# Kernel tuning notes

Hardware: AMD Instinct MI355X
Metric: run time of the kernel (lower is better)

The kernel has to match this reference:

```python
import jax, jax.numpy as jnp
import numpy as np

BS, N, NP, K = 2, 4096, 1024, 8   # batch, fine pts, coarse pts, in-degree per fine node
CI, CO, MID = 32, 16, 32          # in channels (16 skip + 16 interpolated), out channels, radial MLP width
E = BS * N * K


def setup_inputs() -> dict:
    key = jax.random.key(0)
    ks = iter(jax.random.split(key, 64))
    nrm = lambda s, sc=1.0: jax.random.normal(next(ks), s, jnp.float32) * sc
    inp = {}
    inp['h0'] = nrm((BS * N, 16, 1))
    inp['h1'] = nrm((BS * N, 16, 3))
    inp['uph0'] = nrm((BS * NP, 16, 1))
    inp['uph1'] = nrm((BS * NP, 16, 3))
    inp['xyz'] = jax.random.uniform(next(ks), (BS, N, 3), jnp.float32)
    inp['xyz_prev'] = jax.random.uniform(next(ks), (BS, NP, 3), jnp.float32)
    dst = jnp.repeat(jnp.arange(BS * N, dtype=jnp.int32), K)
    src = (dst // N) * N + jax.random.randint(next(ks), (E,), 0, N, jnp.int32)
    inp['edge_src'], inp['edge_dst'] = src, dst
    xf = inp['xyz'].reshape(BS * N, 3)
    inp['r'] = jnp.linalg.norm(xf[src] - xf[dst], axis=-1, keepdims=True)
    # CG basis tensors basis[din,dout]: [E, 2*dout+1, 2*din+1, 2*min(din,dout)+1]
    inp['basis00'] = nrm((E, 1, 1, 1))
    inp['basis01'] = nrm((E, 3, 1, 1))
    inp['basis10'] = nrm((E, 1, 3, 1))
    inp['basis11'] = nrm((E, 3, 3, 3))
    for p, f in (('00', 1), ('01', 1), ('10', 1), ('11', 3)):
        inp['rw1_' + p] = nrm((1, MID), 0.5)
        inp['rb1_' + p] = jnp.zeros((MID,), jnp.float32)
        inp['rw2_' + p] = nrm((MID, MID), 0.2)
        inp['rb2_' + p] = jnp.zeros((MID,), jnp.float32)
        inp['rw3_' + p] = nrm((MID, CO * CI * f), 0.1)
    inp['wself0'] = nrm((CO, CI), 0.1)
    inp['wself1'] = nrm((CO, CI), 0.1)
    inp['gamma0'] = jnp.ones((CO,), jnp.float32)
    inp['beta0'] = jnp.zeros((CO,), jnp.float32)
    inp['gamma1'] = jnp.ones((CO,), jnp.float32)
    inp['beta1'] = jnp.zeros((CO,), jnp.float32)
    return inp


def _radial(r, w1, b1, w2, b2, w3, f):
    x = jax.nn.relu(r @ w1 + b1)
    x = jax.nn.relu(x @ w2 + b2)
    return (x @ w3).reshape(E, CO, CI, f)


def _pair_msg(basis, hsrc, R):
    # basis [E,mo,mi,f], hsrc [E,ci,mi], R [E,co,ci,f] -> msg [E,co,mo]
    # (fused form of per-edge kernel = sum_f R*basis followed by kernel @ src)
    tmp = jnp.einsum('emnf,ein->eimf', basis, hsrc)
    return jnp.einsum('eoif,eimf->eom', R, tmp)


def _gnorm(h, gamma, beta):
    # GNormSE3: norm over m-dim, LayerNorm+ReLU on norms, rescale phase
    n = jnp.sqrt(jnp.sum(h * h, -1) + 1e-12)           # [Nn,co]
    phase = h / n[..., None]
    mu = jnp.mean(n, -1, keepdims=True)
    var = jnp.var(n, -1, keepdims=True)
    t = jax.nn.relu((n - mu) / jnp.sqrt(var + 1e-5) * gamma + beta)
    return t[..., None] * phase


def _fwd(h0, h1, uph0, uph1, xyz, xyz_prev, r, basis00, basis01, basis10, basis11,
         rw1_00, rb1_00, rw2_00, rb2_00, rw3_00,
         rw1_01, rb1_01, rw2_01, rb2_01, rw3_01,
         rw1_10, rb1_10, rw2_10, rb2_10, rw3_10,
         rw1_11, rb1_11, rw2_11, rb2_11, rw3_11,
         wself0, wself1, gamma0, beta0, gamma1, beta1, edge_src, edge_dst):
    # --- three_nn + inverse-squared-distance interpolation of coarse features ---
    d2 = jnp.sum((xyz[:, :, None, :] - xyz_prev[:, None, :, :]) ** 2, -1)  # [B,N,NP]
    negd, idx = jax.lax.top_k(-d2, 3)
    dist = jnp.sqrt(jnp.maximum(-negd, 0.0))
    d2c = jnp.maximum(dist * dist, 1e-10)
    inv = 1.0 / (d2c + 1e-8)
    w = inv / jnp.sum(inv, -1, keepdims=True)          # [B,N,3]

    def interp(uph):
        C, F = uph.shape[1], uph.shape[2]
        fp = uph.reshape(BS, NP, C * F)
        g = jax.vmap(lambda f_, i_: f_[i_])(fp, idx)   # [B,N,3,C*F]
        return jnp.sum(g * w[..., None], 2).reshape(BS * N, C, F)

    h0c = jnp.concatenate([interp(uph0), h0], 1)       # [BN,CI,1]
    h1c = jnp.concatenate([interp(uph1), h1], 1)       # [BN,CI,3]

    # --- GConvSE3: per-edge CG-basis kernels, mean aggregation, self-interaction ---
    hs0, hs1 = h0c[edge_src], h1c[edge_src]
    R00 = _radial(r, rw1_00, rb1_00, rw2_00, rb2_00, rw3_00, 1)
    R01 = _radial(r, rw1_01, rb1_01, rw2_01, rb2_01, rw3_01, 1)
    R10 = _radial(r, rw1_10, rb1_10, rw2_10, rb2_10, rw3_10, 1)
    R11 = _radial(r, rw1_11, rb1_11, rw2_11, rb2_11, rw3_11, 3)
    msg0 = _pair_msg(basis00, hs0, R00) + _pair_msg(basis10, hs1, R10)  # [E,CO,1]
    msg1 = _pair_msg(basis01, hs0, R01) + _pair_msg(basis11, hs1, R11)  # [E,CO,3]
    agg0 = jax.ops.segment_sum(msg0, edge_dst, num_segments=BS * N) / K  # mean (in-degree K)
    agg1 = jax.ops.segment_sum(msg1, edge_dst, num_segments=BS * N) / K
    out0 = agg0 + jnp.einsum('oi,nim->nom', wself0, h0c)
    out1 = agg1 + jnp.einsum('oi,nim->nom', wself1, h1c)

    return _gnorm(out0, gamma0, beta0), _gnorm(out1, gamma1, beta1)


def reference(h0, h1, uph0, uph1, xyz, xyz_prev, r, basis00, basis01, basis10, basis11,
              rw1_00, rb1_00, rw2_00, rb2_00, rw3_00,
              rw1_01, rb1_01, rw2_01, rb2_01, rw3_01,
              rw1_10, rb1_10, rw2_10, rb2_10, rw3_10,
              rw1_11, rb1_11, rw2_11, rb2_11, rw3_11,
              wself0, wself1, gamma0, beta0, gamma1, beta1, edge_src, edge_dst):
    return _fwd(h0, h1, uph0, uph1, xyz, xyz_prev, r, basis00, basis01, basis10, basis11,
                rw1_00, rb1_00, rw2_00, rb2_00, rw3_00,
                rw1_01, rb1_01, rw2_01, rb2_01, rw3_01,
                rw1_10, rb1_10, rw2_10, rb2_10, rw3_10,
                rw1_11, rb1_11, rw2_11, rb2_11, rw3_11,
                wself0, wself1, gamma0, beta0, gamma1, beta1, edge_src, edge_dst)
```

## Files before the change

### kernel.cpp

```cpp
#include <hip/hip_runtime.h>
#include <hip/hip_bf16.h>
#include <hip/hip_fp16.h>
#include <math.h>

#define NPP   1024
#define BN    8192
#define NE    65536

typedef __attribute__((ext_vector_type(8))) short bf16x8;
typedef __attribute__((ext_vector_type(4))) float f32x4;

__device__ __forceinline__ short f2bf(float f) {
  __hip_bfloat16 h = __float2bfloat16(f);
  return *reinterpret_cast<short*>(&h);
}
__device__ __forceinline__ float b2f(short h) {
  unsigned u = ((unsigned)(unsigned short)h) << 16;
  return __uint_as_float(u);
}
__device__ __forceinline__ unsigned short f2h(float f) {
  __half h = __float2half(f);
  return *reinterpret_cast<unsigned short*>(&h);
}
__device__ __forceinline__ float h2f(unsigned short u) {
  __half h = *reinterpret_cast<__half*>(&u);
  return __half2float(h);
}

__device__ __forceinline__ unsigned long long pkkey(float d, int j) {
  return ((unsigned long long)__float_as_uint(d) << 32) | (unsigned int)j;
}

__global__ __launch_bounds__(256) void prolog_kernel(
    const float* __restrict__ h0, const float* __restrict__ h1,
    const float* __restrict__ uph0, const float* __restrict__ uph1,
    const float* __restrict__ xyz, const float* __restrict__ xyzp,
    float* __restrict__ h0c, float* __restrict__ h1c,
    const float* __restrict__ w00, const float* __restrict__ w01,
    const float* __restrict__ w10, const float* __restrict__ w11,
    const float* __restrict__ w2_00, const float* __restrict__ w2_01,
    const float* __restrict__ w2_10, const float* __restrict__ w2_11,
    unsigned short* __restrict__ B00, unsigned short* __restrict__ B01,
    unsigned short* __restrict__ B10, unsigned short* __restrict__ B11,
    unsigned short* __restrict__ W2H, unsigned short* __restrict__ W2L)
{
  const int tid = threadIdx.x;
  if (blockIdx.x >= BN/4) {
    int idx = (blockIdx.x - BN/4) * 256 + tid;
    if (idx < 49152) {
      int a = idx & 16383;
      int i = a & 31, o = (a >> 5) & 15, k = a >> 9;
      int src = k*512 + o*32 + i;
      if (idx < 16384)      B00[a] = (unsigned short)f2bf(w00[src]);
      else if (idx < 32768) B01[a] = (unsigned short)f2bf(w01[src]);
      else                  B10[a] = (unsigned short)f2bf(w10[src]);
    } else if (idx < 98304) {
      int a = idx - 49152;
      int i = a & 31, o = (a >> 5) & 15, s = a >> 9;
      int f = s >> 5, k = s & 31;
      B11[a] = (unsigned short)f2bf(w11[k*1536 + (o*32+i)*3 + f]);
    } else if (idx < 102400) {
      int a = idx - 98304;
      int p = a >> 10, rem = a & 1023;
      int b = rem >> 5, aa = rem & 31;
      const float* w2p = p==0?w2_00 : p==1?w2_01 : p==2?w2_10 : w2_11;
      W2H[a] = (unsigned short)f2bf(w2p[aa*32 + b]);
    } else if (idx < 106496) {
      int a = idx - 102400;
      int p = a >> 10, rem = a & 1023;
      int b = rem >> 5, aa = rem & 31;
      const float* w2p = p==0?w2_00 : p==1?w2_01 : p==2?w2_10 : w2_11;
      float v = w2p[aa*32 + b];
      short h = f2bf(v);
      W2L[a] = (unsigned short)f2bf(v - b2f(h));
    }
    return;
  }

  const int lane = tid & 63;
  const int wid  = tid >> 6;
  const int fi   = blockIdx.x * 4 + wid;
  const int b    = fi >> 12;

  const float px = xyz[fi*3+0], py = xyz[fi*3+1], pz = xyz[fi*3+2];

  unsigned long long k0 = ~0ull, k1 = ~0ull, k2 = ~0ull;
  const float* cbase = xyzp + (size_t)b*NPP*3;
  #pragma unroll 4
  for (int j = lane; j < NPP; j += 64) {
    const float* cp = cbase + j*3;
    float ax = px - cp[0], ay = py - cp[1], az = pz - cp[2];
    float dd = fmaf(az, az, fmaf(ay, ay, ax*ax));
    unsigned long long kk = pkkey(dd, j);
    if (kk < k0)      { k2 = k1; k1 = k0; k0 = kk; }
    else if (kk < k1) { k2 = k1; k1 = kk; }
    else if (kk < k2) { k2 = kk; }
  }
  #pragma unroll
  for (int off = 1; off < 64; off <<= 1) {
    unsigned long long b0 = __shfl_xor(k0, off);
    unsigned long long b1 = __shfl_xor(k1, off);
    unsigned long long b2 = __shfl_xor(k2, off);
    unsigned long long c0, c1, c2;
    if (k0 <= b0) {
      c0 = k0;
      if (k1 <= b0) { c1 = k1; c2 = (k2 <= b0) ? k2 : b0; }
      else          { c1 = b0; c2 = (k1 <= b1) ? k1 : b1; }
    } else {
      c0 = b0;
      if (b1 <= k0) { c1 = b1; c2 = (b2 <= k0) ? b2 : k0; }
      else          { c1 = k0; c2 = (b1 <= k1) ? b1 : k1; }
    }
    k0 = c0; k1 = c1; k2 = c2;
  }
  const int i0 = (int)(k0 & 0xffffffffu);
  const int i1 = (int)(k1 & 0xffffffffu);
  const int i2 = (int)(k2 & 0xffffffffu);
  const float dd0 = __uint_as_float((unsigned)(k0 >> 32));
  const float dd1 = __uint_as_float((unsigned)(k1 >> 32));
  const float dd2 = __uint_as_float((unsigned)(k2 >> 32));

  float w0, w1v, w2v;
  {
    float s0 = sqrtf(fmaxf(dd0, 0.f));
    float s1 = sqrtf(fmaxf(dd1, 0.f));
    float s2 = sqrtf(fmaxf(dd2, 0.f));
    w0  = 1.f / (fmaxf(s0*s0, 1e-10f) + 1e-8f);
    w1v = 1.f / (fmaxf(s1*s1, 1e-10f) + 1e-8f);
    w2v = 1.f / (fmaxf(s2*s2, 1e-10f) + 1e-8f);
    float wsum = w0 + w1v + w2v;
    w0 /= wsum; w1v /= wsum; w2v /= wsum;
  }

  const float* u0 = uph0 + (size_t)b*NPP*16;
  const float* u1 = uph1 + (size_t)b*NPP*48;
  if (lane < 16) {
    int c = lane;
    h0c[(size_t)fi*32 + c] = w0*u0[i0*16+c] + w1v*u0[i1*16+c] + w2v*u0[i2*16+c];
    h0c[(size_t)fi*32 + 16 + c] = h0[(size_t)fi*16 + c];
  } else {
    int q = lane - 16;
    h1c[(size_t)fi*96 + q] = w0*u1[i0*48+q] + w1v*u1[i1*48+q] + w2v*u1[i2*48+q];
    h1c[(size_t)fi*96 + 48 + q] = h1[(size_t)fi*48 + q];
  }
}

struct EP {
  const float *r; const int *esrc;
  const float *b00, *b01, *b10, *b11;
  const float *w1_00, *b1_00, *b2_00;
  const float *w1_01, *b1_01, *b2_01;
  const float *w1_10, *b1_10, *b2_10;
  const float *w1_11, *b1_11, *b2_11;
  const unsigned short *B00, *B01, *B10, *B11, *W2H, *W2L;
  const float *h0c, *h1c;
  float *agg0, *agg1;
};

#define CVT4(PTR) ({ ushort4 u_ = *(const ushort4*)(PTR); \
    f32x4 r_; r_[0]=h2f(u_.x); r_[1]=h2f(u_.y); r_[2]=h2f(u_.z); r_[3]=h2f(u_.w); r_; })

__global__ __launch_bounds__(256) void edge_mfma(EP P)
{
  __shared__ __align__(16) unsigned short x2Lh[32*264];

  const int tid  = threadIdx.x;
  const int wid  = tid >> 6;
  const int lane = tid & 63;
  const int el   = lane & 15;
  const int kg   = lane >> 4;
  const int kg4  = kg << 2;
  const int eb   = blockIdx.x * 64 + wid * 16;
  const int e    = eb + el;
  const int isl  = kg * 8;

  const int   sidx = P.esrc[e];
  const float rv   = P.r[e];

  const f32x4 zero4 = {0.f, 0.f, 0.f, 0.f};

  #pragma unroll
  for (int p = 0; p < 4; ++p) {
    const float* w1p = p==0?P.w1_00 : p==1?P.w1_01 : p==2?P.w1_10 : P.w1_11;
    const float* b1p = p==0?P.b1_00 : p==1?P.b1_01 : p==2?P.b1_10 : P.b1_11;
    const float* b2p = p==0?P.b2_00 : p==1?P.b2_01 : p==2?P.b2_10 : P.b2_11;
    const unsigned short* w2hp = P.W2H + p*1024;
    const unsigned short* w2lp = P.W2L + p*1024;
    f32x4 wa  = *(const f32x4*)(w1p + isl);
    f32x4 wb  = *(const f32x4*)(w1p + isl + 4);
    f32x4 ba  = *(const f32x4*)(b1p + isl);
    f32x4 bbv = *(const f32x4*)(b1p + isl + 4);
    bf16x8 bh0 = *(const bf16x8*)(w2hp + el*32 + isl);
    bf16x8 bh1 = *(const bf16x8*)(w2hp + (16+el)*32 + isl);
    bf16x8 bl0 = *(const bf16x8*)(w2lp + el*32 + isl);
    bf16x8 bl1 = *(const bf16x8*)(w2lp + (16+el)*32 + isl);
    float b2v0 = b2p[el];
    float b2v1 = b2p[16 + el];
    bf16x8 axh, axl;
    #pragma unroll
    for (int j = 0; j < 4; ++j) {
      float v0 = fmaxf(fmaf(rv, wa[j], ba[j]),  0.f);
      float v1 = fmaxf(fmaf(rv, wb[j], bbv[j]), 0.f);
      short h0s = f2bf(v0), h1s_ = f2bf(v1);
      axh[j]   = h0s;  axl[j]   = f2bf(v0 - b2f(h0s));
      axh[j+4] = h1s_; axl[j+4] = f2bf(v1 - b2f(h1s_));
    }
    f32x4 z0 = __builtin_amdgcn_mfma_f32_16x16x32_bf16(axl, bh0, zero4, 0,0,0);
    z0 = __builtin_amdgcn_mfma_f32_16x16x32_bf16(axh, bl0, z0, 0,0,0);
    z0 = __builtin_amdgcn_mfma_f32_16x16x32_bf16(axh, bh0, z0, 0,0,0);
    f32x4 z1 = __builtin_amdgcn_mfma_f32_16x16x32_bf16(axl, bh1, zero4, 0,0,0);
    z1 = __builtin_amdgcn_mfma_f32_16x16x32_bf16(axh, bl1, z1, 0,0,0);
    z1 = __builtin_amdgcn_mfma_f32_16x16x32_bf16(axh, bh1, z1, 0,0,0);
    ushort4 o0, o1v;
    o0.x  = f2h(fmaxf(z0[0] + b2v0, 0.f));
    o0.y  = f2h(fmaxf(z0[1] + b2v0, 0.f));
    o0.z  = f2h(fmaxf(z0[2] + b2v0, 0.f));
    o0.w  = f2h(fmaxf(z0[3] + b2v0, 0.f));
    o1v.x = f2h(fmaxf(z1[0] + b2v1, 0.f));
    o1v.y = f2h(fmaxf(z1[1] + b2v1, 0.f));
    o1v.z = f2h(fmaxf(z1[2] + b2v1, 0.f));
    o1v.w = f2h(fmaxf(z1[3] + b2v1, 0.f));
    *(ushort4*)&x2Lh[el*264      + wid*64 + p*16 + kg4] = o0;
    *(ushort4*)&x2Lh[(16+el)*264 + wid*64 + p*16 + kg4] = o1v;
  }

  f32x4 h0a = *(const f32x4*)(P.h0c + (size_t)sidx*32 + isl);
  f32x4 h0b = *(const f32x4*)(P.h0c + (size_t)sidx*32 + isl + 4);
  float h1sl[24];
  {
    const float* hp = P.h1c + (size_t)sidx*96 + isl*3;
    #pragma unroll
    for (int q = 0; q < 6; ++q) {
      f32x4 v = *(const f32x4*)(hp + q*4);
      h1sl[q*4+0]=v[0]; h1sl[q*4+1]=v[1]; h1sl[q*4+2]=v[2]; h1sl[q*4+3]=v[3];
    }
  }

  bf16x8 a_h0;
  #pragma unroll
  for (int j = 0; j < 4; ++j) { a_h0[j] = f2bf(h0a[j]); a_h0[j+4] = f2bf(h0b[j]); }

  const int xrow = wid*64 + kg4;

  f32x4 macc0 = zero4;
  {
    const unsigned short* bb = P.B00 + el*32 + isl;
    #pragma unroll 4
    for (int t = 0; t < 32; ++t) {
      bf16x8 bv = *(const bf16x8*)(bb + t*512);
      f32x4 z = __builtin_amdgcn_mfma_f32_16x16x32_bf16(a_h0, bv, zero4, 0, 0, 0);
      f32x4 xs = CVT4(&x2Lh[t*264 + xrow + 0]);
      macc0[0] = fmaf(xs[0], z[0], macc0[0]);
      macc0[1] = fmaf(xs[1], z[1], macc0[1]);
      macc0[2] = fmaf(xs[2], z[2], macc0[2]);
      macc0[3] = fmaf(xs[3], z[3], macc0[3]);
    }
  }
  {
    f32x4 bv = *(const f32x4*)(P.b00 + eb + kg4);
    macc0[0]*=bv[0]; macc0[1]*=bv[1]; macc0[2]*=bv[2]; macc0[3]*=bv[3];
  }

  {
    const float* bp = P.b10 + (size_t)e*3;
    float c0 = bp[0], c1 = bp[1], c2 = bp[2];
    bf16x8 a_t;
    #pragma unroll
    for (int j = 0; j < 8; ++j)
      a_t[j] = f2bf(c0*h1sl[j*3+0] + c1*h1sl[j*3+1] + c2*h1sl[j*3+2]);
    const unsigned short* bb = P.B10 + el*32 + isl;
    #pragma unroll 4
    for (int t = 0; t < 32; ++t) {
      bf16x8 bv = *(const bf16x8*)(bb + t*512);
      f32x4 z = __builtin_amdgcn_mfma_f32_16x16x32_bf16(a_t, bv, zero4, 0, 0, 0);
      f32x4 xs = CVT4(&x2Lh[t*264 + xrow + 32]);
      macc0[0] = fmaf(xs[0], z[0], macc0[0]);
      macc0[1] = fmaf(xs[1], z[1], macc0[1]);
      macc0[2] = fmaf(xs[2], z[2], macc0[2]);
      macc0[3] = fmaf(xs[3], z[3], macc0[3]);
    }
  }
  {
    float s = macc0[0]+macc0[1]+macc0[2]+macc0[3];
    s += __shfl_xor(s, 16);
    if ((kg & 1) == 0)
      P.agg0[(size_t)((eb >> 3) + (kg >> 1))*16 + el] = s * 0.125f;
  }

  f32x4 c01 = zero4;
  {
    const unsigned short* bb = P.B01 + el*32 + isl;
    #pragma unroll 4
    for (int t = 0; t < 32; ++t) {
      bf16x8 bv = *(const bf16x8*)(bb + t*512);
      f32x4 z = __builtin_amdgcn_mfma_f32_16x16x32_bf16(a_h0, bv, zero4, 0, 0, 0);
      f32x4 xs = CVT4(&x2Lh[t*264 + xrow + 16]);
      c01[0] = fmaf(xs[0], z[0], c01[0]);
      c01[1] = fmaf(xs[1], z[1], c01[1]);
      c01[2] = fmaf(xs[2], z[2], c01[2]);
      c01[3] = fmaf(xs[3], z[3], c01[3]);
    }
  }
  f32x4 m1a, m1b, m1c;
  {
    const float* bp = P.b01 + (size_t)(eb + kg4)*3;
    f32x4 q0 = *(const f32x4*)(bp);
    f32x4 q1 = *(const f32x4*)(bp + 4);
    f32x4 q2 = *(const f32x4*)(bp + 8);
    m1a[0]=c01[0]*q0[0]; m1a[1]=c01[1]*q0[3]; m1a[2]=c01[2]*q1[2]; m1a[3]=c01[3]*q2[1];
    m1b[0]=c01[0]*q0[1]; m1b[1]=c01[1]*q1[0]; m1b[2]=c01[2]*q1[3]; m1b[3]=c01[3]*q2[2];
    m1c[0]=c01[0]*q0[2]; m1c[1]=c01[1]*q1[1]; m1c[2]=c01[2]*q2[0]; m1c[3]=c01[3]*q2[3];
  }

  {
    const float* b11e = P.b11 + (size_t)e*27;
    #pragma unroll 1
    for (int f = 0; f < 3; ++f) {
      float bm[9];
      #pragma unroll
      for (int mn = 0; mn < 9; ++mn) bm[mn] = b11e[mn*3 + f];
      bf16x8 am0, am1, am2;
      #pragma unroll
      for (int j = 0; j < 8; ++j) {
        float hn0 = h1sl[j*3+0], hn1 = h1sl[j*3+1], hn2 = h1sl[j*3+2];
        am0[j] = f2bf(bm[0]*hn0 + bm[1]*hn1 + bm[2]*hn2);
        am1[j] = f2bf(bm[3]*hn0 + bm[4]*hn1 + bm[5]*hn2);
        am2[j] = f2bf(bm[6]*hn0 + bm[7]*hn1 + bm[8]*hn2);
      }
      const unsigned short* bb = P.B11 + (size_t)f*16384 + el*32 + isl;
      #pragma unroll 4
      for (int t = 0; t < 32; ++t) {
        bf16x8 bv = *(const bf16x8*)(bb + t*512);
        f32x4 z0 = __builtin_amdgcn_mfma_f32_16x16x32_bf16(am0, bv, zero4, 0, 0, 0);
        f32x4 z1 = __builtin_amdgcn_mfma_f32_16x16x32_bf16(am1, bv, zero4, 0, 0, 0);
        f32x4 z2 = __builtin_amdgcn_mfma_f32_16x16x32_bf16(am2, bv, zero4, 0, 0, 0);
        f32x4 xs = CVT4(&x2Lh[t*264 + xrow + 48]);
        m1a[0] = fmaf(xs[0], z0[0], m1a[0]);
        m1a[1] = fmaf(xs[1], z0[1], m1a[1]);
        m1a[2] = fmaf(xs[2], z0[2], m1a[2]);
        m1a[3] = fmaf(xs[3], z0[3], m1a[3]);
        m1b[0] = fmaf(xs[0], z1[0], m1b[0]);
        m1b[1] = fmaf(xs[1], z1[1], m1b[1]);
        m1b[2] = fmaf(xs[2], z1[2], m1b[2]);
        m1b[3] = fmaf(xs[3], z1[3], m1b[3]);
        m1c[0] = fmaf(xs[0], z2[0], m1c[0]);
        m1c[1] = fmaf(xs[1], z2[1], m1c[1]);
        m1c[2] = fmaf(xs[2], z2[2], m1c[2]);
        m1c[3] = fmaf(xs[3], z2[3], m1c[3]);
      }
    }
  }

  {
    float sa = m1a[0]+m1a[1]+m1a[2]+m1a[3]; sa += __shfl_xor(sa, 16);
    float sb = m1b[0]+m1b[1]+m1b[2]+m1b[3]; sb += __shfl_xor(sb, 16);
    float sc = m1c[0]+m1c[1]+m1c[2]+m1c[3]; sc += __shfl_xor(sc, 16);
    if ((kg & 1) == 0) {
      float* p = P.agg1 + (size_t)((eb >> 3) + (kg >> 1))*48 + el*3;
      p[0] = sa * 0.125f; p[1] = sb * 0.125f; p[2] = sc * 0.125f;
    }
  }
}

__global__ __launch_bounds__(256) void gnorm_kernel(
    const float* __restrict__ agg0, const float* __restrict__ agg1,
    const float* __restrict__ h0c, const float* __restrict__ h1c,
    const float* __restrict__ ws0, const float* __restrict__ ws1,
    const float* __restrict__ g0, const float* __restrict__ be0,
    const float* __restrict__ g1, const float* __restrict__ be1,
    float* __restrict__ out)
{
  const int gt  = blockIdx.x * 256 + threadIdx.x;
  const int fi  = gt >> 2;
  const int t4  = gt & 3;
  const int ob  = t4 * 4;

  const float* h0p = h0c + (size_t)fi*32;
  const float* h1p = h1c + (size_t)fi*96;

  float o0[4];
  #pragma unroll
  for (int oo = 0; oo < 4; ++oo) {
    int o = ob + oo;
    float a = agg0[(size_t)fi*16 + o];
    #pragma unroll
    for (int i = 0; i < 32; ++i)
      a = fmaf(ws0[o*32+i], h0p[i], a);
    o0[oo] = a;
  }
  {
    float n0[4], lmu = 0.f;
    #pragma unroll
    for (int oo = 0; oo < 4; ++oo) { n0[oo] = sqrtf(fmaf(o0[oo], o0[oo], 1e-12f)); lmu += n0[oo]; }
    lmu += __shfl_xor(lmu, 1); lmu += __shfl_xor(lmu, 2);
    float mu = lmu * 0.0625f;
    float lv = 0.f;
    #pragma unroll
    for (int oo = 0; oo < 4; ++oo) { float d = n0[oo]-mu; lv = fmaf(d, d, lv); }
    lv += __shfl_xor(lv, 1); lv += __shfl_xor(lv, 2);
    float inv = 1.f / sqrtf(lv * 0.0625f + 1e-5f);
    #pragma unroll
    for (int oo = 0; oo < 4; ++oo) {
      int o = ob + oo;
      float t = fmaxf(fmaf((n0[oo]-mu)*inv, g0[o], be0[o]), 0.f);
      out[(size_t)fi*16 + o] = t * (o0[oo] / n0[oo]);
    }
  }

  float o1[12];
  #pragma unroll
  for (int oo = 0; oo < 4; ++oo) {
    int o = ob + oo;
    float a0 = agg1[(size_t)fi*48 + o*3+0];
    float a1 = agg1[(size_t)fi*48 + o*3+1];
    float a2 = agg1[(size_t)fi*48 + o*3+2];
    #pragma unroll
    for (int i = 0; i < 32; ++i) {
      float wv = ws1[o*32+i];
      a0 = fmaf(wv, h1p[i*3+0], a0);
      a1 = fmaf(wv, h1p[i*3+1], a1);
      a2 = fmaf(wv, h1p[i*3+2], a2);
    }
    o1[oo*3+0] = a0; o1[oo*3+1] = a1; o1[oo*3+2] = a2;
  }
  {
    float n1[4], lmu = 0.f;
    #pragma unroll
    for (int oo = 0; oo < 4; ++oo) {
      float s = fmaf(o1[oo*3+0], o1[oo*3+0], 1e-12f);
      s = fmaf(o1[oo*3+1], o1[oo*3+1], s);
      s = fmaf(o1[oo*3+2], o1[oo*3+2], s);
      n1[oo] = sqrtf(s); lmu += n1[oo];
    }
    lmu += __shfl_xor(lmu, 1); lmu += __shfl_xor(lmu, 2);
    float mu = lmu * 0.0625f;
    float lv = 0.f;
    #pragma unroll
    for (int oo = 0; oo < 4; ++oo) { float d = n1[oo]-mu; lv = fmaf(d, d, lv); }
    lv += __shfl_xor(lv, 1); lv += __shfl_xor(lv, 2);
    float inv = 1.f / sqrtf(lv * 0.0625f + 1e-5f);
    float* out1 = out + (size_t)BN*16;
    #pragma unroll
    for (int oo = 0; oo < 4; ++oo) {
      int o = ob + oo;
      float t = fmaxf(fmaf((n1[oo]-mu)*inv, g1[o], be1[o]), 0.f);
      #pragma unroll
      for (int m = 0; m < 3; ++m)
        out1[(size_t)fi*48 + o*3+m] = t * (o1[oo*3+m] / n1[oo]);
    }
  }
}

extern "C" void kernel_launch(void* const* d_in, const int* in_sizes, int n_in,
                              void* d_out, int out_size, void* d_ws, size_t ws_size,
                              hipStream_t stream)
{
  (void)in_sizes; (void)n_in; (void)out_size; (void)ws_size;
  const float* h0   = (const float*)d_in[0];
  const float* h1   = (const float*)d_in[1];
  const float* uph0 = (const float*)d_in[2];
  const float* uph1 = (const float*)d_in[3];
  const float* xyz  = (const float*)d_in[4];
  const float* xyzp = (const float*)d_in[5];
  const int*   esrc = (const int*)d_in[6];
  const float* rr   = (const float*)d_in[8];

  float* wsp  = (float*)d_ws;
  float* h0c  = wsp;
  float* h1c  = h0c + (size_t)BN*32;
  float* agg0 = h1c + (size_t)BN*96;
  float* agg1 = agg0 + (size_t)BN*16;
  unsigned short* B00 = (unsigned short*)(agg1 + (size_t)BN*48);
  unsigned short* B01 = B00 + 16384;
  unsigned short* B10 = B01 + 16384;
  unsigned short* B11 = B10 + 16384;
  unsigned short* W2H = B11 + 49152;
  unsigned short* W2L = W2H + 4096;

  prolog_kernel<<<BN/4 + 416, 256, 0, stream>>>(
      h0, h1, uph0, uph1, xyz, xyzp, h0c, h1c,
      (const float*)d_in[17], (const float*)d_in[22],
      (const float*)d_in[27], (const float*)d_in[32],
      (const float*)d_in[15], (const float*)d_in[20],
      (const float*)d_in[25], (const float*)d_in[30],
      B00, B01, B10, B11, W2H, W2L);

  EP P;
  P.r = rr; P.esrc = esrc;
  P.b00 = (const float*)d_in[9];  P.b01 = (const float*)d_in[10];
  P.b10 = (const float*)d_in[11]; P.b11 = (const float*)d_in[12];
  P.w1_00 = (const float*)d_in[13]; P.b1_00 = (const float*)d_in[14]; P.b2_00 = (const float*)d_in[16];
  P.w1_01 = (const float*)d_in[18]; P.b1_01 = (const float*)d_in[19]; P.b2_01 = (const float*)d_in[21];
  P.w1_10 = (const float*)d_in[23]; P.b1_10 = (const float*)d_in[24]; P.b2_10 = (const float*)d_in[26];
  P.w1_11 = (const float*)d_in[28]; P.b1_11 = (const float*)d_in[29]; P.b2_11 = (const float*)d_in[31];
  P.B00 = B00; P.B01 = B01; P.B10 = B10; P.B11 = B11; P.W2H = W2H; P.W2L = W2L;
  P.h0c = h0c; P.h1c = h1c; P.agg0 = agg0; P.agg1 = agg1;

  edge_mfma<<<NE/64, 256, 0, stream>>>(P);

  gnorm_kernel<<<BN*4/256, 256, 0, stream>>>(agg0, agg1, h0c, h1c,
      (const float*)d_in[33], (const float*)d_in[34],
      (const float*)d_in[35], (const float*)d_in[36],
      (const float*)d_in[37], (const float*)d_in[38],
      (float*)d_out);
}
```

Baseline: 103.2 us.

## Fuse per-pair MFMA loops to share x2 reads and raise MFMA ILP

The three separate t-loops for the 00, 01 and 10 pairs are merged into one loop that issues three independent MFMAs per iteration. The three f-iterations of the 11 pair are also folded into a single t-loop that keeps nine A operands in registers and runs nine MFMAs per step. This removes repeated loop overhead and dependent MFMA-to-FMA chains, and exposes more independent MFMAs to hide latency. In exchange it raises register pressure (nine bf16x8 operands plus more accumulators), which could lower occupancy or cause spills.

```diff
diff --git a/kernel.cpp b/kernel.cpp
--- a/kernel.cpp
+++ b/kernel.cpp
@@ -240,67 +240,58 @@
   #pragma unroll
   for (int j = 0; j < 4; ++j) { a_h0[j] = f2bf(h0a[j]); a_h0[j+4] = f2bf(h0b[j]); }
 
-  const int xrow = wid*64 + kg4;
-
-  f32x4 macc0 = zero4;
-  {
-    const unsigned short* bb = P.B00 + el*32 + isl;
-    #pragma unroll 4
-    for (int t = 0; t < 32; ++t) {
-      bf16x8 bv = *(const bf16x8*)(bb + t*512);
-      f32x4 z = __builtin_amdgcn_mfma_f32_16x16x32_bf16(a_h0, bv, zero4, 0, 0, 0);
-      f32x4 xs = CVT4(&x2Lh[t*264 + xrow + 0]);
-      macc0[0] = fmaf(xs[0], z[0], macc0[0]);
-      macc0[1] = fmaf(xs[1], z[1], macc0[1]);
-      macc0[2] = fmaf(xs[2], z[2], macc0[2]);
-      macc0[3] = fmaf(xs[3], z[3], macc0[3]);
-    }
-  }
-  {
-    f32x4 bv = *(const f32x4*)(P.b00 + eb + kg4);
-    macc0[0]*=bv[0]; macc0[1]*=bv[1]; macc0[2]*=bv[2]; macc0[3]*=bv[3];
-  }
-
+  bf16x8 a_t;
   {
     const float* bp = P.b10 + (size_t)e*3;
     float c0 = bp[0], c1 = bp[1], c2 = bp[2];
-    bf16x8 a_t;
     #pragma unroll
     for (int j = 0; j < 8; ++j)
       a_t[j] = f2bf(c0*h1sl[j*3+0] + c1*h1sl[j*3+1] + c2*h1sl[j*3+2]);
-    const unsigned short* bb = P.B10 + el*32 + isl;
-    #pragma unroll 4
+  }
+
+  const int xrow = wid*64 + kg4;
+
+  f32x4 macc00 = zero4, c01 = zero4, macc10 = zero4;
+  {
+    const unsigned short* bb00 = P.B00 + el*32 + isl;
+    const unsigned short* bb01 = P.B01 + el*32 + isl;
+    const unsigned short* bb10 = P.B10 + el*32 + isl;
+    #pragma unroll 2
     for (int t = 0; t < 32; ++t) {
-      bf16x8 bv = *(const bf16x8*)(bb + t*512);
-      f32x4 z = __builtin_amdgcn_mfma_f32_16x16x32_bf16(a_t, bv, zero4, 0, 0, 0);
-      f32x4 xs = CVT4(&x2Lh[t*264 + xrow + 32]);
-      macc0[0] = fmaf(xs[0], z[0], macc0[0]);
-      macc0[1] = fmaf(xs[1], z[1], macc0[1]);
-      macc0[2] = fmaf(xs[2], z[2], macc0[2]);
-      macc0[3] = fmaf(xs[3], z[3], macc0[3]);
-    }
-  }
-  {
-    float s = macc0[0]+macc0[1]+macc0[2]+macc0[3];
+      bf16x8 bv00 = *(const bf16x8*)(bb00 + t*512);
+      bf16x8 bv01 = *(const bf16x8*)(bb01 + t*512);
+      bf16x8 bv10 = *(const bf16x8*)(bb10 + t*512);
+      f32x4 xs0 = CVT4(&x2Lh[t*264 + xrow + 0]);
+      f32x4 xs1 = CVT4(&x2Lh[t*264 + xrow + 16]);
+      f32x4 xs2 = CVT4(&x2Lh[t*264 + xrow + 32]);
+      f32x4 z00 = __builtin_amdgcn_mfma_f32_16x16x32_bf16(a_h0, bv00, zero4, 0, 0, 0);
+      f32x4 z01 = __builtin_amdgcn_mfma_f32_16x16x32_bf16(a_h0, bv01, zero4, 0, 0, 0);
+      f32x4 z10 = __builtin_amdgcn_mfma_f32_16x16x32_bf16(a_t,  bv10, zero4, 0, 0, 0);
+      macc00[0] = fmaf(xs0[0], z00[0], macc00[0]);
+      macc00[1] = fmaf(xs0[1], z00[1], macc00[1]);
+      macc00[2] = fmaf(xs0[2], z00[2], macc00[2]);
+      macc00[3] = fmaf(xs0[3], z00[3], macc00[3]);
+      c01[0] = fmaf(xs1[0], z01[0], c01[0]);
+      c01[1] = fmaf(xs1[1], z01[1], c01[1]);
+      c01[2] = fmaf(xs1[2], z01[2], c01[2]);
+      c01[3] = fmaf(xs1[3], z01[3], c01[3]);
+      macc10[0] = fmaf(xs2[0], z10[0], macc10[0]);
+      macc10[1] = fmaf(xs2[1], z10[1], macc10[1]);
+      macc10[2] = fmaf(xs2[2], z10[2], macc10[2]);
+      macc10[3] = fmaf(xs2[3], z10[3], macc10[3]);
+    }
+  }
+  {
+    f32x4 bv = *(const f32x4*)(P.b00 + eb + kg4);
+    float s = fmaf(bv[0], macc00[0], macc10[0])
+            + fmaf(bv[1], macc00[1], macc10[1])
+            + fmaf(bv[2], macc00[2], macc10[2])
+            + fmaf(bv[3], macc00[3], macc10[3]);
     s += __shfl_xor(s, 16);
     if ((kg & 1) == 0)
       P.agg0[(size_t)((eb >> 3) + (kg >> 1))*16 + el] = s * 0.125f;
   }
 
-  f32x4 c01 = zero4;
-  {
-    const unsigned short* bb = P.B01 + el*32 + isl;
-    #pragma unroll 4
-    for (int t = 0; t < 32; ++t) {
-      bf16x8 bv = *(const bf16x8*)(bb + t*512);
-      f32x4 z = __builtin_amdgcn_mfma_f32_16x16x32_bf16(a_h0, bv, zero4, 0, 0, 0);
-      f32x4 xs = CVT4(&x2Lh[t*264 + xrow + 16]);
-      c01[0] = fmaf(xs[0], z[0], c01[0]);
-      c01[1] = fmaf(xs[1], z[1], c01[1]);
-      c01[2] = fmaf(xs[2], z[2], c01[2]);
-      c01[3] = fmaf(xs[3], z[3], c01[3]);
-    }
-  }
   f32x4 m1a, m1b, m1c;
   {
     const float* bp = P.b01 + (size_t)(eb + kg4)*3;
@@ -313,28 +304,34 @@
   }
 
   {
+    bf16x8 am[3][3];
     const float* b11e = P.b11 + (size_t)e*27;
-    #pragma unroll 1
+    #pragma unroll
     for (int f = 0; f < 3; ++f) {
       float bm[9];
       #pragma unroll
       for (int mn = 0; mn < 9; ++mn) bm[mn] = b11e[mn*3 + f];
-      bf16x8 am0, am1, am2;
       #pragma unroll
       for (int j = 0; j < 8; ++j) {
         float hn0 = h1sl[j*3+0], hn1 = h1sl[j*3+1], hn2 = h1sl[j*3+2];
-        am0[j] = f2bf(bm[0]*hn0 + bm[1]*hn1 + bm[2]*hn2);
-        am1[j] = f2bf(bm[3]*hn0 + bm[4]*hn1 + bm[5]*hn2);
-        am2[j] = f2bf(bm[6]*hn0 + bm[7]*hn1 + bm[8]*hn2);
+        am[f][0][j] = f2bf(bm[0]*hn0 + bm[1]*hn1 + bm[2]*hn2);
+        am[f][1][j] = f2bf(bm[3]*hn0 + bm[4]*hn1 + bm[5]*hn2);
+        am[f][2][j] = f2bf(bm[6]*hn0 + bm[7]*hn1 + bm[8]*hn2);
       }
-      const unsigned short* bb = P.B11 + (size_t)f*16384 + el*32 + isl;
-      #pragma unroll 4
-      for (int t = 0; t < 32; ++t) {
-        bf16x8 bv = *(const bf16x8*)(bb + t*512);
-        f32x4 z0 = __builtin_amdgcn_mfma_f32_16x16x32_bf16(am0, bv, zero4, 0, 0, 0);
-        f32x4 z1 = __builtin_amdgcn_mfma_f32_16x16x32_bf16(am1, bv, zero4, 0, 0, 0);
-        f32x4 z2 = __builtin_amdgcn_mfma_f32_16x16x32_bf16(am2, bv, zero4, 0, 0, 0);
-        f32x4 xs = CVT4(&x2Lh[t*264 + xrow + 48]);
+    }
+    const unsigned short* bb = P.B11 + el*32 + isl;
+    #pragma unroll 4
+    for (int t = 0; t < 32; ++t) {
+      bf16x8 bv0 = *(const bf16x8*)(bb + t*512);
+      bf16x8 bv1 = *(const bf16x8*)(bb + 16384 + t*512);
+      bf16x8 bv2 = *(const bf16x8*)(bb + 32768 + t*512);
+      f32x4 xs = CVT4(&x2Lh[t*264 + xrow + 48]);
+      #pragma unroll
+      for (int f = 0; f < 3; ++f) {
+        bf16x8 bv = f==0 ? bv0 : (f==1 ? bv1 : bv2);
+        f32x4 z0 = __builtin_amdgcn_mfma_f32_16x16x32_bf16(am[f][0], bv, zero4, 0, 0, 0);
+        f32x4 z1 = __builtin_amdgcn_mfma_f32_16x16x32_bf16(am[f][1], bv, zero4, 0, 0, 0);
+        f32x4 z2 = __builtin_amdgcn_mfma_f32_16x16x32_bf16(am[f][2], bv, zero4, 0, 0, 0);
         m1a[0] = fmaf(xs[0], z0[0], m1a[0]);
         m1a[1] = fmaf(xs[1], z0[1], m1a[1]);
         m1a[2] = fmaf(xs[2], z0[2], m1a[2]);
```

Result: no change. 101.5 us (median of 2 runs) (-1.6%).
